# Kernel optimization log

Hardware: AMD Instinct MI355X
Metric: run time of the kernel (lower is better)

## Reference

```python
import jax, jax.numpy as jnp
import numpy as np

BIGNET_DIM = 1024
GROUP = 16
N_LIN = 15  # 6 blocks (last has no LN after) x 3 QLoRALinear
N_LN = 5
LORA_SCALE = 0.125  # 1/8
LN_EPS = 1e-5


def setup_inputs() -> dict:
    key = jax.random.key(0)
    ks = jax.random.split(key, 8)
    B = 8192
    x = jax.random.normal(ks[0], (B, BIGNET_DIM), dtype=jnp.float32)
    # 4-bit codes in [0, 16), group-wise fp16 scales (absmax-like, positive)
    q_w = jax.random.randint(ks[1], (N_LIN, BIGNET_DIM, BIGNET_DIM), 0, 16, dtype=jnp.int32)
    scales = (jax.random.uniform(ks[2], (N_LIN, BIGNET_DIM, BIGNET_DIM // GROUP)) * 0.05 + 0.01).astype(jnp.float16)
    biases = (jax.random.normal(ks[3], (N_LIN, BIGNET_DIM)) * 0.01).astype(jnp.float16)
    lora_A = jax.random.normal(ks[4], (N_LIN, 32, BIGNET_DIM), dtype=jnp.float32) * (1.0 / np.sqrt(BIGNET_DIM))
    # lora_B is zero-init in the module; use small random values so the LoRA path is exercised
    lora_B = jax.random.normal(ks[5], (N_LIN, BIGNET_DIM, 32), dtype=jnp.float32) * 0.01
    ln_g = jnp.ones((N_LN, BIGNET_DIM), dtype=jnp.float32)
    ln_b = jnp.zeros((N_LN, BIGNET_DIM), dtype=jnp.float32)
    return {"x": x, "q_w": q_w, "scales": scales, "biases": biases,
            "lora_A": lora_A, "lora_B": lora_B, "ln_g": ln_g, "ln_b": ln_b}


def _dequant4bit(q, scale):
    # q: [out, in] int codes in [0,16); scale: [out, in//GROUP] fp16
    # w = (q / 15 * 2 - 1) * group_scale, computed in fp16 like the torch code
    s = jnp.repeat(scale, GROUP, axis=1)  # [out, in]
    return (q.astype(jnp.float16) * jnp.float16(2.0 / 15.0) - jnp.float16(1.0)) * s


def _qlora_linear(x, q, scale, bias, A, B):
    w = _dequant4bit(q, scale)                                   # [out, in] f16
    half = jnp.dot(x.astype(jnp.float16), w.T) + bias            # f16 GEMM
    lora = jnp.dot(jnp.dot(x, A.T), B.T) * LORA_SCALE            # f32 rank-32 path
    return half.astype(jnp.float32) + lora


def _layernorm(x, g, b):
    mu = jnp.mean(x, axis=-1, keepdims=True)
    var = jnp.mean(jnp.square(x - mu), axis=-1, keepdims=True)
    return (x - mu) * jax.lax.rsqrt(var + LN_EPS) * g + b


def _forward(x, q_w, scales, biases, lora_A, lora_B, ln_g, ln_b):
    h = x
    li = 0
    for blk in range(6):
        r = h
        for j in range(3):
            r = _qlora_linear(r, q_w[li], scales[li], biases[li], lora_A[li], lora_B[li])
            li += 1
            if j < 2:
                r = jax.nn.relu(r)
        h = r + h  # block residual
        if blk < 5:
            h = _layernorm(h, ln_g[blk], ln_b[blk])
    return h


def reference(x, q_w, scales, biases, lora_A, lora_B, ln_g, ln_b):
    return _forward(x, q_w, scales, biases, lora_A, lora_B, ln_g, ln_b)
```

## Files before the change

kernel.cpp:

```cpp
#include <hip/hip_runtime.h>

typedef _Float16 f16;
typedef _Float16 f16x8 __attribute__((ext_vector_type(8)));
typedef _Float16 f16x4 __attribute__((ext_vector_type(4)));
typedef float f32x4 __attribute__((ext_vector_type(4)));

__global__ void detect_kernel(const unsigned short* __restrict__ sc, int* __restrict__ mode)
{
    if (threadIdx.x != 0 || blockIdx.x != 0) return;
    bool ok16 = true, okbf = true;
    for (int i = 0; i < 64; i++) {
        const unsigned short b = sc[i];
        union { unsigned short u; f16 h; } ch; ch.u = b;
        const float fv = (float)ch.h;
        if (!(fv > 0.008f && fv < 0.062f)) ok16 = false;
        union { unsigned int u; float f; } cb; cb.u = ((unsigned int)b) << 16;
        if (!(cb.f > 0.008f && cb.f < 0.062f)) okbf = false;
    }
    *mode = ok16 ? 0 : (okbf ? 1 : 2);
}

__device__ __forceinline__ float load_half_like(const void* p, int i, int mode)
{
    if (mode == 0) return (float)((const f16*)p)[i];
    if (mode == 1) {
        union { unsigned int u; float f; } c;
        c.u = ((unsigned int)((const unsigned short*)p)[i]) << 16;
        return c.f;
    }
    return ((const float*)p)[i];
}

__global__ void prep_kernel(const float* __restrict__ x, const int* __restrict__ qw,
                            const void* __restrict__ scales, const void* __restrict__ biases,
                            const float* __restrict__ lA, const float* __restrict__ lB,
                            const int* __restrict__ modep,
                            f16* __restrict__ Wdq, f16* __restrict__ A16,
                            f16* __restrict__ B16, f16* __restrict__ x16,
                            float* __restrict__ bias32)
{
    const int bid = blockIdx.x, tid = threadIdx.x;
    if (bid < 3840) {
        const int md = *modep;
        const int g = bid * 256 + tid;
        const float s = load_half_like(scales, g, md);
        const int4* qp = (const int4*)(qw + (size_t)g * 16);
        f16x8 w0, w1;
        #pragma unroll
        for (int v = 0; v < 4; v++) {
            const int4 q4 = qp[v];
            const int qs[4] = {q4.x, q4.y, q4.z, q4.w};
            #pragma unroll
            for (int j = 0; j < 4; j++) {
                f16 t = (f16)qs[j];
                t = t * (f16)(2.0f / 15.0f);
                t = t - (f16)1.0f;
                const f16 w = (f16)((float)t * s);
                if (v < 2) w0[v * 4 + j] = w; else w1[(v - 2) * 4 + j] = w;
            }
        }
        *(f16x8*)(Wdq + (size_t)g * 16) = w0;
        *(f16x8*)(Wdq + (size_t)g * 16 + 8) = w1;
    } else if (bid < 4320) {
        const int i = (bid - 3840) * 1024 + tid * 4;
        const float4 a = *(const float4*)(lA + i);
        f16x4 o = {(f16)a.x, (f16)a.y, (f16)a.z, (f16)a.w};
        *(f16x4*)(A16 + i) = o;
    } else if (bid < 4800) {
        const int i = (bid - 4320) * 1024 + tid * 4;
        const float4 a = *(const float4*)(lB + i);
        f16x4 o = {(f16)(0.125f * a.x), (f16)(0.125f * a.y),
                   (f16)(0.125f * a.z), (f16)(0.125f * a.w)};
        *(f16x4*)(B16 + i) = o;
    } else if (bid < 12992) {
        const int i = (bid - 4800) * 1024 + tid * 4;
        const float4 a = *(const float4*)(x + i);
        f16x4 o = {(f16)a.x, (f16)a.y, (f16)a.z, (f16)a.w};
        *(f16x4*)(x16 + i) = o;
    } else {
        const int md = *modep;
        const int i = (bid - 12992) * 1024 + tid * 4;
        float4 o;
        o.x = load_half_like(biases, i, md);
        o.y = load_half_like(biases, i + 1, md);
        o.z = load_half_like(biases, i + 2, md);
        o.w = load_half_like(biases, i + 3, md);
        *(float4*)(bias32 + i) = o;
    }
}

__device__ __forceinline__ void gl_lds16(const f16* g, f16* l)
{
    __builtin_amdgcn_global_load_lds(
        (const __attribute__((address_space(1))) void*)g,
        (__attribute__((address_space(3))) void*)l, 16, 0, 0);
}

__global__ __launch_bounds__(256, 2)
void layer_kernel(const f16* __restrict__ X16, const f16* __restrict__ W,
                  const f16* __restrict__ AL, const f16* __restrict__ BL,
                  const float* __restrict__ biasL, const float* __restrict__ resid,
                  float* __restrict__ out32, f16* __restrict__ out16, int do_relu)
{
    __shared__ __align__(16) f16 lds[36864];

    const int tid  = threadIdx.x;
    const int lane = tid & 63;
    const int wv   = tid >> 6;
    const int wy   = wv >> 1, wx = wv & 1;
    const int by   = blockIdx.x & 63;
    const int bx   = blockIdx.x >> 6;
    const int row0 = by << 7;
    const int col0 = bx << 7;

    const int lr = lane >> 3;
    const int pc = lane & 7;
    const int gksw = ((pc ^ lr) << 3);

    const int m15 = lane & 15;
    const int q2  = lane >> 4;
    const int sw  = m15 & 7;
    const int po0 = ((q2 ^ sw) << 3);
    const int po1 = (((4 + q2) ^ sw) << 3);
    const int q8  = q2 << 3;

    f32x4 acc[4][4] = {};
    f32x4 tacc[2][2] = {};

    auto stage = [&](f16* buf, int kt) {
        const int kb = (kt << 6) + gksw;
        #pragma unroll
        for (int i = 0; i < 4; i++) {
            gl_lds16(X16 + (size_t)(row0 + wv * 32 + i * 8 + lr) * 1024 + kb,
                     buf + (wv * 32 + i * 8) * 64);
            gl_lds16(W + (size_t)(col0 + wv * 32 + i * 8 + lr) * 1024 + kb,
                     buf + 8192 + (wv * 32 + i * 8) * 64);
        }
        gl_lds16(AL + (size_t)(wv * 8 + lr) * 1024 + kb,
                 buf + 16384 + wv * 8 * 64);
    };

    stage(lds, 0);

    for (int kt = 0; kt < 16; kt++) {
        __syncthreads();
        const f16* cur = lds + (kt & 1) * 18432;
        const f16* sA = cur;
        const f16* sB = cur + 8192;
        const f16* sL = cur + 16384;

        if (kt < 15) stage(lds + ((kt + 1) & 1) * 18432, kt + 1);

        f16x8 af[2][4], bf[2][4], lf[2][2];
        #pragma unroll
        for (int s = 0; s < 2; s++) {
            const int po = s ? po1 : po0;
            #pragma unroll
            for (int mi = 0; mi < 4; mi++)
                af[s][mi] = *(const f16x8*)(sA + (wy * 64 + mi * 16 + m15) * 64 + po);
            #pragma unroll
            for (int ni = 0; ni < 4; ni++)
                bf[s][ni] = *(const f16x8*)(sB + (wx * 64 + ni * 16 + m15) * 64 + po);
            #pragma unroll
            for (int pi = 0; pi < 2; pi++)
                lf[s][pi] = *(const f16x8*)(sL + (pi * 16 + m15) * 64 + po);
        }

        #pragma unroll
        for (int s = 0; s < 2; s++) {
            #pragma unroll
            for (int mi = 0; mi < 4; mi++)
                #pragma unroll
                for (int ni = 0; ni < 4; ni++)
                    acc[mi][ni] = __builtin_amdgcn_mfma_f32_16x16x32_f16(af[s][mi], bf[s][ni], acc[mi][ni], 0, 0, 0);
            #pragma unroll
            for (int mi = 0; mi < 2; mi++)
                #pragma unroll
                for (int pi = 0; pi < 2; pi++)
                    tacc[mi][pi] = __builtin_amdgcn_mfma_f32_16x16x32_f16(af[s][2 * wx + mi], lf[s][pi], tacc[mi][pi], 0, 0, 0);
        }
    }

    __syncthreads();
    float* Tl = (float*)lds;
    const int q4 = (lane >> 4) << 2;
    {
        #pragma unroll
        for (int mi = 0; mi < 2; mi++)
            #pragma unroll
            for (int pi = 0; pi < 2; pi++)
                #pragma unroll
                for (int r = 0; r < 4; r++)
                    Tl[(wy * 64 + wx * 32 + mi * 16 + q4 + r) * 33 + pi * 16 + m15] = tacc[mi][pi][r];
    }
    __syncthreads();

    f16x8 tf[4];
    #pragma unroll
    for (int mi = 0; mi < 4; mi++) {
        const float* tp = Tl + (wy * 64 + mi * 16 + m15) * 33 + q8;
        f16x8 v;
        #pragma unroll
        for (int j = 0; j < 8; j++) v[j] = (f16)tp[j];
        tf[mi] = v;
    }
    f16x8 bfr[4]; float bb[4];
    #pragma unroll
    for (int ni = 0; ni < 4; ni++) {
        const int colg = col0 + wx * 64 + ni * 16 + m15;
        bfr[ni] = *(const f16x8*)(BL + (size_t)colg * 32 + q8);
        bb[ni] = biasL[colg];
    }
    #pragma unroll
    for (int mi = 0; mi < 4; mi++)
        #pragma unroll
        for (int ni = 0; ni < 4; ni++) {
            #pragma unroll
            for (int r = 0; r < 4; r++)
                acc[mi][ni][r] += bb[ni];
            acc[mi][ni] = __builtin_amdgcn_mfma_f32_16x16x32_f16(tf[mi], bfr[ni], acc[mi][ni], 0, 0, 0);
        }

    __syncthreads();
    if (out16) {
        f16* ot = lds;
        #pragma unroll
        for (int mi = 0; mi < 4; mi++)
            #pragma unroll
            for (int ni = 0; ni < 4; ni++)
                #pragma unroll
                for (int r = 0; r < 4; r++) {
                    float v = acc[mi][ni][r];
                    if (do_relu) v = fmaxf(v, 0.0f);
                    ot[(wy * 64 + mi * 16 + q4 + r) * 136 + wx * 64 + ni * 16 + m15] = (f16)v;
                }
        __syncthreads();
        const int rr = tid >> 4;
        const int cc = (tid & 15) << 3;
        #pragma unroll
        for (int it = 0; it < 8; it++) {
            const int r = it * 16 + rr;
            const f16x8 v = *(const f16x8*)(ot + r * 136 + cc);
            *(f16x8*)(out16 + (size_t)(row0 + r) * 1024 + col0 + cc) = v;
        }
    } else {
        float* otf = (float*)lds;
        const int rr = tid >> 5;
        const int cc = (tid & 31) << 2;
        #pragma unroll
        for (int half = 0; half < 2; half++) {
            if (wy == half) {
                #pragma unroll
                for (int mi = 0; mi < 4; mi++)
                    #pragma unroll
                    for (int ni = 0; ni < 4; ni++)
                        #pragma unroll
                        for (int r = 0; r < 4; r++)
                            otf[(mi * 16 + q4 + r) * 140 + wx * 64 + ni * 16 + m15] = acc[mi][ni][r];
            }
            __syncthreads();
            #pragma unroll
            for (int it = 0; it < 8; it++) {
                const int r = it * 8 + rr;
                f32x4 v = *(const f32x4*)(otf + r * 140 + cc);
                const size_t gidx = (size_t)(row0 + half * 64 + r) * 1024 + col0 + cc;
                const f32x4 rs = *(const f32x4*)(resid + gidx);
                v += rs;
                *(f32x4*)(out32 + gidx) = v;
            }
            if (half == 0) __syncthreads();
        }
    }
}

__global__ void ln_kernel(float* __restrict__ h, f16* __restrict__ h16,
                          const float* __restrict__ g, const float* __restrict__ b)
{
    const int row = blockIdx.x, tid = threadIdx.x;
    float* hp = h + (size_t)row * 1024;
    const int c = tid * 4;
    const float4 v = *(const float4*)(hp + c);
    float s = v.x + v.y + v.z + v.w;
    #pragma unroll
    for (int off = 32; off > 0; off >>= 1) s += __shfl_down(s, off);
    __shared__ float r1[4], r2[4];
    const int wv = tid >> 6, lane = tid & 63;
    if (lane == 0) r1[wv] = s;
    __syncthreads();
    const float mu = (r1[0] + r1[1] + r1[2] + r1[3]) * (1.0f / 1024.0f);
    const float dx = v.x - mu, dy = v.y - mu, dz = v.z - mu, dw = v.w - mu;
    float s2 = dx * dx + dy * dy + dz * dz + dw * dw;
    #pragma unroll
    for (int off = 32; off > 0; off >>= 1) s2 += __shfl_down(s2, off);
    if (lane == 0) r2[wv] = s2;
    __syncthreads();
    const float var = (r2[0] + r2[1] + r2[2] + r2[3]) * (1.0f / 1024.0f);
    const float rs = 1.0f / sqrtf(var + 1e-5f);
    float4 o;
    o.x = dx * rs * g[c]     + b[c];
    o.y = dy * rs * g[c + 1] + b[c + 1];
    o.z = dz * rs * g[c + 2] + b[c + 2];
    o.w = dw * rs * g[c + 3] + b[c + 3];
    *(float4*)(hp + c) = o;
    f16x4 o16 = {(f16)o.x, (f16)o.y, (f16)o.z, (f16)o.w};
    *(f16x4*)(h16 + (size_t)row * 1024 + c) = o16;
}

extern "C" void kernel_launch(void* const* d_in, const int* in_sizes, int n_in,
                              void* d_out, int out_size, void* d_ws, size_t ws_size,
                              hipStream_t stream)
{
    const float* x      = (const float*)d_in[0];
    const int*   qw     = (const int*)d_in[1];
    const void*  scales = d_in[2];
    const void*  biases = d_in[3];
    const float* lA     = (const float*)d_in[4];
    const float* lB     = (const float*)d_in[5];
    const float* lng    = (const float*)d_in[6];
    const float* lnb    = (const float*)d_in[7];
    float* out = (float*)d_out;

    char* ws = (char*)d_ws;
    int*   mode   = (int*)(ws);
    float* bias32 = (float*)(ws + 64);
    f16* Wdq = (f16*)(ws + 65536u);
    f16* A16 = (f16*)(ws + 31522816u);
    f16* B16 = (f16*)(ws + 32505856u);
    f16* fA  = (f16*)(ws + 33488896u);
    f16* fB  = (f16*)(ws + 50266112u);
    float* h32 = out;

    detect_kernel<<<1, 64, 0, stream>>>((const unsigned short*)scales, mode);
    prep_kernel<<<13007, 256, 0, stream>>>(x, qw, scales, biases, lA, lB, mode,
                                           Wdq, A16, B16, fA, bias32);

    int li = 0;
    for (int blk = 0; blk < 6; blk++) {
        const float* resid = (blk == 0) ? x : h32;
        for (int j = 0; j < 3; j++, li++) {
            const int wl = li < 15 ? li : 14;
            const f16* in16 = (j == 1) ? fB : fA;
            f16* o16 = (j == 0) ? fB : (j == 1 ? fA : (f16*)nullptr);
            float* o32 = nullptr;
            const float* rz = nullptr;
            if (j == 2) { o32 = h32; rz = resid; }
            layer_kernel<<<512, 256, 0, stream>>>(in16,
                Wdq + (size_t)wl * 1048576,
                A16 + (size_t)wl * 32768,
                B16 + (size_t)wl * 32768,
                bias32 + (size_t)wl * 1024,
                rz, o32, o16, j < 2 ? 1 : 0);
        }
        if (blk < 5)
            ln_kernel<<<8192, 256, 0, stream>>>(h32, fA, lng + blk * 1024, lnb + blk * 1024);
    }
}
```

Before: 1.380 ms.

## Use triple-buffered BK=32 LDS pipeline with direct LoRA-A register loads

Restructures the GEMM main loop from double-buffered 64-wide K tiles to triple-buffered 32-wide tiles, prefetching two stages ahead. Waits use explicit vmcnt counts and a raw s_barrier instead of __syncthreads. The LoRA A fragments now load straight from global memory into registers, double-buffered across iterations, rather than being staged through LDS. This is meant to shrink LDS use (more room for occupancy) and hide load latency better, at the cost of hand-tuned waitcnt values that must exactly match the number of outstanding loads.

```diff
diff --git a/kernel.cpp b/kernel.cpp
--- a/kernel.cpp
+++ b/kernel.cpp
@@ -102,7 +102,7 @@
                   const float* __restrict__ biasL, const float* __restrict__ resid,
                   float* __restrict__ out32, f16* __restrict__ out16, int do_relu)
 {
-    __shared__ __align__(16) f16 lds[36864];
+    __shared__ __align__(16) f16 lds[24576];
 
     const int tid  = threadIdx.x;
     const int lane = tid & 63;
@@ -113,72 +113,79 @@
     const int row0 = by << 7;
     const int col0 = bx << 7;
 
-    const int lr = lane >> 3;
-    const int pc = lane & 7;
-    const int gksw = ((pc ^ lr) << 3);
+    const int lr4 = lane >> 2;
+    const int csw = (((lane & 3) ^ (lr4 & 3)) << 3);
 
     const int m15 = lane & 15;
     const int q2  = lane >> 4;
-    const int sw  = m15 & 7;
-    const int po0 = ((q2 ^ sw) << 3);
-    const int po1 = (((4 + q2) ^ sw) << 3);
+    const int po  = ((q2 ^ (m15 & 3)) << 3);
     const int q8  = q2 << 3;
 
     f32x4 acc[4][4] = {};
     f32x4 tacc[2][2] = {};
-
-    auto stage = [&](f16* buf, int kt) {
-        const int kb = (kt << 6) + gksw;
-        #pragma unroll
-        for (int i = 0; i < 4; i++) {
-            gl_lds16(X16 + (size_t)(row0 + wv * 32 + i * 8 + lr) * 1024 + kb,
-                     buf + (wv * 32 + i * 8) * 64);
-            gl_lds16(W + (size_t)(col0 + wv * 32 + i * 8 + lr) * 1024 + kb,
-                     buf + 8192 + (wv * 32 + i * 8) * 64);
-        }
-        gl_lds16(AL + (size_t)(wv * 8 + lr) * 1024 + kb,
-                 buf + 16384 + wv * 8 * 64);
+    f16x8 lfA[2], lfB[2];
+
+    auto stage = [&](int kt, int bsel) {
+        f16* buf = lds + bsel * 8192;
+        const int kb = (kt << 5) + csw;
+        #pragma unroll
+        for (int i = 0; i < 2; i++) {
+            gl_lds16(X16 + (size_t)(row0 + wv * 32 + i * 16 + lr4) * 1024 + kb,
+                     buf + (wv * 32 + i * 16) * 32);
+            gl_lds16(W   + (size_t)(col0 + wv * 32 + i * 16 + lr4) * 1024 + kb,
+                     buf + 4096 + (wv * 32 + i * 16) * 32);
+        }
     };
 
-    stage(lds, 0);
-
-    for (int kt = 0; kt < 16; kt++) {
-        __syncthreads();
-        const f16* cur = lds + (kt & 1) * 18432;
-        const f16* sA = cur;
-        const f16* sB = cur + 8192;
-        const f16* sL = cur + 16384;
-
-        if (kt < 15) stage(lds + ((kt + 1) & 1) * 18432, kt + 1);
-
-        f16x8 af[2][4], bf[2][4], lf[2][2];
-        #pragma unroll
-        for (int s = 0; s < 2; s++) {
-            const int po = s ? po1 : po0;
-            #pragma unroll
-            for (int mi = 0; mi < 4; mi++)
-                af[s][mi] = *(const f16x8*)(sA + (wy * 64 + mi * 16 + m15) * 64 + po);
+    stage(0, 0);
+    asm volatile("" ::: "memory");
+    lfA[0] = *(const f16x8*)(AL + (size_t)m15 * 1024 + q8);
+    lfA[1] = *(const f16x8*)(AL + (size_t)(16 + m15) * 1024 + q8);
+    asm volatile("" ::: "memory");
+    stage(1, 1);
+
+    auto body = [&](int kt, f16x8 (&lfc)[2], f16x8 (&lfn)[2]) {
+        if (kt < 31) asm volatile("s_waitcnt vmcnt(6)" ::: "memory");
+        else         asm volatile("s_waitcnt vmcnt(2)" ::: "memory");
+        __builtin_amdgcn_s_barrier();
+        if (kt < 31) {
+            const int kb2 = ((kt + 1) << 5) + q8;
+            lfn[0] = *(const f16x8*)(AL + (size_t)m15 * 1024 + kb2);
+            lfn[1] = *(const f16x8*)(AL + (size_t)(16 + m15) * 1024 + kb2);
+        }
+        asm volatile("" ::: "memory");
+        __builtin_amdgcn_sched_barrier(0);
+        if (kt < 30) stage(kt + 2, (kt + 2) % 3);
+        __builtin_amdgcn_sched_barrier(0);
+        const f16* sA = lds + (kt % 3) * 8192;
+        const f16* sB = sA + 4096;
+        f16x8 af[4], bf[4];
+        #pragma unroll
+        for (int mi = 0; mi < 4; mi++)
+            af[mi] = *(const f16x8*)(sA + (wy * 64 + mi * 16 + m15) * 32 + po);
+        #pragma unroll
+        for (int ni = 0; ni < 4; ni++)
+            bf[ni] = *(const f16x8*)(sB + (wx * 64 + ni * 16 + m15) * 32 + po);
+        if (kt < 30)       asm volatile("s_waitcnt vmcnt(10) lgkmcnt(0)" ::: "memory");
+        else if (kt == 30) asm volatile("s_waitcnt vmcnt(6) lgkmcnt(0)" ::: "memory");
+        else               asm volatile("s_waitcnt vmcnt(0) lgkmcnt(0)" ::: "memory");
+        __builtin_amdgcn_sched_barrier(0);
+        #pragma unroll
+        for (int mi = 0; mi < 4; mi++)
             #pragma unroll
             for (int ni = 0; ni < 4; ni++)
-                bf[s][ni] = *(const f16x8*)(sB + (wx * 64 + ni * 16 + m15) * 64 + po);
+                acc[mi][ni] = __builtin_amdgcn_mfma_f32_16x16x32_f16(af[mi], bf[ni], acc[mi][ni], 0, 0, 0);
+        #pragma unroll
+        for (int mi = 0; mi < 2; mi++)
             #pragma unroll
             for (int pi = 0; pi < 2; pi++)
-                lf[s][pi] = *(const f16x8*)(sL + (pi * 16 + m15) * 64 + po);
-        }
-
-        #pragma unroll
-        for (int s = 0; s < 2; s++) {
-            #pragma unroll
-            for (int mi = 0; mi < 4; mi++)
-                #pragma unroll
-                for (int ni = 0; ni < 4; ni++)
-                    acc[mi][ni] = __builtin_amdgcn_mfma_f32_16x16x32_f16(af[s][mi], bf[s][ni], acc[mi][ni], 0, 0, 0);
-            #pragma unroll
-            for (int mi = 0; mi < 2; mi++)
-                #pragma unroll
-                for (int pi = 0; pi < 2; pi++)
-                    tacc[mi][pi] = __builtin_amdgcn_mfma_f32_16x16x32_f16(af[s][2 * wx + mi], lf[s][pi], tacc[mi][pi], 0, 0, 0);
-        }
+                tacc[mi][pi] = __builtin_amdgcn_mfma_f32_16x16x32_f16(af[2 * wx + mi], lfc[pi], tacc[mi][pi], 0, 0, 0);
+    };
+
+    #pragma unroll
+    for (int k2 = 0; k2 < 16; k2++) {
+        body(2 * k2,     lfA, lfB);
+        body(2 * k2 + 1, lfB, lfA);
     }
 
     __syncthreads();
```

Result: slower. 1.463 ms (+6.0%).

## Replace LDS-staged GEMM mainloop with direct global-to-register double-buffered fragment loads

Applied to the files above, without the earlier changes.

The GEMM main loop no longer stages X, W and LoRA-A tiles through double-buffered LDS with global_load_lds and barriers. Each wave now loads its MFMA fragments straight from global memory into registers, double-buffered across k-steps. LDS shrinks to the epilogue's needs, which removes barriers in the loop and LDS read traffic. The cost is that data shared between waves is no longer reused, so global/L2 traffic goes up (each A row is fetched by two waves and each B row by two). The loads are also 16-byte strided accesses with less coalescing, and register pressure rises.

```diff
diff --git a/kernel.cpp b/kernel.cpp
--- a/kernel.cpp
+++ b/kernel.cpp
@@ -89,20 +89,13 @@
     }
 }
 
-__device__ __forceinline__ void gl_lds16(const f16* g, f16* l)
-{
-    __builtin_amdgcn_global_load_lds(
-        (const __attribute__((address_space(1))) void*)g,
-        (__attribute__((address_space(3))) void*)l, 16, 0, 0);
-}
-
 __global__ __launch_bounds__(256, 2)
 void layer_kernel(const f16* __restrict__ X16, const f16* __restrict__ W,
                   const f16* __restrict__ AL, const f16* __restrict__ BL,
                   const float* __restrict__ biasL, const float* __restrict__ resid,
                   float* __restrict__ out32, f16* __restrict__ out16, int do_relu)
 {
-    __shared__ __align__(16) f16 lds[36864];
+    __shared__ __align__(16) f16 lds[18176];
 
     const int tid  = threadIdx.x;
     const int lane = tid & 63;
@@ -113,75 +106,54 @@
     const int row0 = by << 7;
     const int col0 = bx << 7;
 
-    const int lr = lane >> 3;
-    const int pc = lane & 7;
-    const int gksw = ((pc ^ lr) << 3);
-
     const int m15 = lane & 15;
     const int q2  = lane >> 4;
-    const int sw  = m15 & 7;
-    const int po0 = ((q2 ^ sw) << 3);
-    const int po1 = (((4 + q2) ^ sw) << 3);
     const int q8  = q2 << 3;
+
+    const f16* Ap = X16 + (size_t)(row0 + wy * 64 + m15) * 1024 + q8;
+    const f16* Bp = W   + (size_t)(col0 + wx * 64 + m15) * 1024 + q8;
+    const f16* Lp = AL  + (size_t)m15 * 1024 + q8;
 
     f32x4 acc[4][4] = {};
     f32x4 tacc[2][2] = {};
 
-    auto stage = [&](f16* buf, int kt) {
-        const int kb = (kt << 6) + gksw;
-        #pragma unroll
-        for (int i = 0; i < 4; i++) {
-            gl_lds16(X16 + (size_t)(row0 + wv * 32 + i * 8 + lr) * 1024 + kb,
-                     buf + (wv * 32 + i * 8) * 64);
-            gl_lds16(W + (size_t)(col0 + wv * 32 + i * 8 + lr) * 1024 + kb,
-                     buf + 8192 + (wv * 32 + i * 8) * 64);
-        }
-        gl_lds16(AL + (size_t)(wv * 8 + lr) * 1024 + kb,
-                 buf + 16384 + wv * 8 * 64);
+    f16x8 afA[4], bfA[4], lfA[2];
+    f16x8 afB[4], bfB[4], lfB[2];
+
+    auto loadset = [&](int kt, f16x8 (&af)[4], f16x8 (&bf)[4], f16x8 (&lf)[2]) {
+        const int kb = kt << 5;
+        #pragma unroll
+        for (int mi = 0; mi < 4; mi++)
+            af[mi] = *(const f16x8*)(Ap + mi * 16384 + kb);
+        #pragma unroll
+        for (int ni = 0; ni < 4; ni++)
+            bf[ni] = *(const f16x8*)(Bp + ni * 16384 + kb);
+        #pragma unroll
+        for (int pi = 0; pi < 2; pi++)
+            lf[pi] = *(const f16x8*)(Lp + pi * 16384 + kb);
     };
-
-    stage(lds, 0);
-
-    for (int kt = 0; kt < 16; kt++) {
-        __syncthreads();
-        const f16* cur = lds + (kt & 1) * 18432;
-        const f16* sA = cur;
-        const f16* sB = cur + 8192;
-        const f16* sL = cur + 16384;
-
-        if (kt < 15) stage(lds + ((kt + 1) & 1) * 18432, kt + 1);
-
-        f16x8 af[2][4], bf[2][4], lf[2][2];
-        #pragma unroll
-        for (int s = 0; s < 2; s++) {
-            const int po = s ? po1 : po0;
-            #pragma unroll
-            for (int mi = 0; mi < 4; mi++)
-                af[s][mi] = *(const f16x8*)(sA + (wy * 64 + mi * 16 + m15) * 64 + po);
+    auto compute = [&](f16x8 (&af)[4], f16x8 (&bf)[4], f16x8 (&lf)[2]) {
+        #pragma unroll
+        for (int mi = 0; mi < 4; mi++)
             #pragma unroll
             for (int ni = 0; ni < 4; ni++)
-                bf[s][ni] = *(const f16x8*)(sB + (wx * 64 + ni * 16 + m15) * 64 + po);
+                acc[mi][ni] = __builtin_amdgcn_mfma_f32_16x16x32_f16(af[mi], bf[ni], acc[mi][ni], 0, 0, 0);
+        #pragma unroll
+        for (int mi = 0; mi < 2; mi++)
             #pragma unroll
             for (int pi = 0; pi < 2; pi++)
-                lf[s][pi] = *(const f16x8*)(sL + (pi * 16 + m15) * 64 + po);
-        }
-
-        #pragma unroll
-        for (int s = 0; s < 2; s++) {
-            #pragma unroll
-            for (int mi = 0; mi < 4; mi++)
-                #pragma unroll
-                for (int ni = 0; ni < 4; ni++)
-                    acc[mi][ni] = __builtin_amdgcn_mfma_f32_16x16x32_f16(af[s][mi], bf[s][ni], acc[mi][ni], 0, 0, 0);
-            #pragma unroll
-            for (int mi = 0; mi < 2; mi++)
-                #pragma unroll
-                for (int pi = 0; pi < 2; pi++)
-                    tacc[mi][pi] = __builtin_amdgcn_mfma_f32_16x16x32_f16(af[s][2 * wx + mi], lf[s][pi], tacc[mi][pi], 0, 0, 0);
-        }
-    }
-
-    __syncthreads();
+                tacc[mi][pi] = __builtin_amdgcn_mfma_f32_16x16x32_f16(af[2 * wx + mi], lf[pi], tacc[mi][pi], 0, 0, 0);
+    };
+
+    loadset(0, afA, bfA, lfA);
+    #pragma unroll
+    for (int k2 = 0; k2 < 16; k2++) {
+        loadset(2 * k2 + 1, afB, bfB, lfB);
+        compute(afA, bfA, lfA);
+        if (k2 < 15) loadset(2 * k2 + 2, afA, bfA, lfA);
+        compute(afB, bfB, lfB);
+    }
+
     float* Tl = (float*)lds;
     const int q4 = (lane >> 4) << 2;
     {
```

Measured after the change: 5.030 ms. 3.64x slower.

## Store activations and weights in K-panel-major layout for contiguous tile loads

Applied to the files above, without the earlier changes.

Activations (x16, h16, out16), dequantized weights and LoRA A are now written in a K-tiled layout of 64-wide panels, so each panel is stored contiguously with rows of 64 halves. The GEMM stage loads then read one contiguous 128-byte row per tile row instead of striding 2 KB between rows. This is meant to improve DRAM/L2 locality and coalescing of the global-to-LDS loads. Every producer and consumer has to agree on the new layout, which raises the risk of an indexing mismatch.

```diff
diff --git a/kernel.cpp b/kernel.cpp
--- a/kernel.cpp
+++ b/kernel.cpp
@@ -4,6 +4,7 @@
 typedef _Float16 f16x8 __attribute__((ext_vector_type(8)));
 typedef _Float16 f16x4 __attribute__((ext_vector_type(4)));
 typedef float f32x4 __attribute__((ext_vector_type(4)));
+
 
 __global__ void detect_kernel(const unsigned short* __restrict__ sc, int* __restrict__ mode)
 {
@@ -59,13 +60,22 @@
                 if (v < 2) w0[v * 4 + j] = w; else w1[(v - 2) * 4 + j] = w;
             }
         }
-        *(f16x8*)(Wdq + (size_t)g * 16) = w0;
-        *(f16x8*)(Wdq + (size_t)g * 16 + 8) = w1;
+        const int row = g >> 6;
+        const int li  = row >> 10;
+        const int col = row & 1023;
+        const int grp = g & 63;
+        const size_t dst = (size_t)li * 1048576 + (size_t)(grp >> 2) * 65536
+                         + (size_t)col * 64 + ((grp & 3) << 4);
+        *(f16x8*)(Wdq + dst) = w0;
+        *(f16x8*)(Wdq + dst + 8) = w1;
     } else if (bid < 4320) {
         const int i = (bid - 3840) * 1024 + tid * 4;
         const float4 a = *(const float4*)(lA + i);
         f16x4 o = {(f16)a.x, (f16)a.y, (f16)a.z, (f16)a.w};
-        *(f16x4*)(A16 + i) = o;
+        const int li = i >> 15, j = i & 32767;
+        const int p = j >> 10, k = j & 1023;
+        *(f16x4*)(A16 + (size_t)li * 32768 + (size_t)(k >> 6) * 2048
+                      + (size_t)p * 64 + (k & 63)) = o;
     } else if (bid < 4800) {
         const int i = (bid - 4320) * 1024 + tid * 4;
         const float4 a = *(const float4*)(lB + i);
@@ -73,10 +83,11 @@
                    (f16)(0.125f * a.z), (f16)(0.125f * a.w)};
         *(f16x4*)(B16 + i) = o;
     } else if (bid < 12992) {
-        const int i = (bid - 4800) * 1024 + tid * 4;
-        const float4 a = *(const float4*)(x + i);
+        const int row = bid - 4800;
+        const int k = tid * 4;
+        const float4 a = *(const float4*)(x + (size_t)row * 1024 + k);
         f16x4 o = {(f16)a.x, (f16)a.y, (f16)a.z, (f16)a.w};
-        *(f16x4*)(x16 + i) = o;
+        *(f16x4*)(x16 + (size_t)(k >> 6) * 524288 + (size_t)row * 64 + (k & 63)) = o;
     } else {
         const int md = *modep;
         const int i = (bid - 12992) * 1024 + tid * 4;
@@ -115,7 +126,7 @@
 
     const int lr = lane >> 3;
     const int pc = lane & 7;
-    const int gksw = ((pc ^ lr) << 3);
+    const int csw = ((pc ^ lr) << 3);
 
     const int m15 = lane & 15;
     const int q2  = lane >> 4;
@@ -128,15 +139,17 @@
     f32x4 tacc[2][2] = {};
 
     auto stage = [&](f16* buf, int kt) {
-        const int kb = (kt << 6) + gksw;
+        const f16* Xt = X16 + (size_t)kt * 524288 + csw;
+        const f16* Wt = W   + (size_t)kt * 65536  + csw;
+        const f16* At = AL  + (size_t)kt * 2048   + csw;
         #pragma unroll
         for (int i = 0; i < 4; i++) {
-            gl_lds16(X16 + (size_t)(row0 + wv * 32 + i * 8 + lr) * 1024 + kb,
+            gl_lds16(Xt + (size_t)(row0 + wv * 32 + i * 8 + lr) * 64,
                      buf + (wv * 32 + i * 8) * 64);
-            gl_lds16(W + (size_t)(col0 + wv * 32 + i * 8 + lr) * 1024 + kb,
+            gl_lds16(Wt + (size_t)(col0 + wv * 32 + i * 8 + lr) * 64,
                      buf + 8192 + (wv * 32 + i * 8) * 64);
         }
-        gl_lds16(AL + (size_t)(wv * 8 + lr) * 1024 + kb,
+        gl_lds16(At + (size_t)(wv * 8 + lr) * 64,
                  buf + 16384 + wv * 8 * 64);
     };
 
@@ -237,11 +250,12 @@
         __syncthreads();
         const int rr = tid >> 4;
         const int cc = (tid & 15) << 3;
+        f16* o0 = out16 + (size_t)(2 * bx + (cc >> 6)) * 524288 + (cc & 63);
         #pragma unroll
         for (int it = 0; it < 8; it++) {
             const int r = it * 16 + rr;
             const f16x8 v = *(const f16x8*)(ot + r * 136 + cc);
-            *(f16x8*)(out16 + (size_t)(row0 + r) * 1024 + col0 + cc) = v;
+            *(f16x8*)(o0 + (size_t)(row0 + r) * 64) = v;
         }
     } else {
         float* otf = (float*)lds;
@@ -303,7 +317,7 @@
     o.w = dw * rs * g[c + 3] + b[c + 3];
     *(float4*)(hp + c) = o;
     f16x4 o16 = {(f16)o.x, (f16)o.y, (f16)o.z, (f16)o.w};
-    *(f16x4*)(h16 + (size_t)row * 1024 + c) = o16;
+    *(f16x4*)(h16 + (size_t)(c >> 6) * 524288 + (size_t)row * 64 + (c & 63)) = o16;
 }
 
 extern "C" void kernel_launch(void* const* d_in, const int* in_sizes, int n_in,
```

After: 1.383 ms. About the same (+0.2%).
